# Kernel optimization log

Measured on AMD Instinct MI355X. Metric: run time of the kernel, lower is better.

Reference implementation:

```python
import jax, jax.numpy as jnp
import numpy as np
import math

K = 2
CAPACITY = -1
NEED_L_AUX = True


def topk_gating(logits, k=K, capacity=CAPACITY, need_l_aux=NEED_L_AUX):
    # logits: (T, P, E) tokens x prototypes x experts-per-prototype
    gates = jax.nn.softmax(logits.astype(jnp.float32), axis=-1).astype(logits.dtype)
    T, P, E = gates.shape
    cap = int(math.ceil(1.25 * T / E)) if capacity < 0 else capacity

    idx1 = jnp.argmax(gates, axis=-1)                      # (T, P)
    mask1 = jax.nn.one_hot(idx1, E, dtype=jnp.int32)       # (T, P, E)
    loc1 = jnp.cumsum(mask1, axis=0) - 1                   # position in expert queue
    if need_l_aux:
        me = jnp.mean(gates, axis=0)
        ce = jnp.mean(mask1.astype(jnp.float32), axis=0)
        l_aux = jnp.mean(me * ce)
    else:
        l_aux = jnp.zeros((), jnp.float32)
    mask1 = mask1 * (loc1 < cap)                           # drop over-capacity tokens
    loc1_s = jnp.sum(loc1 * mask1, axis=-1)                # (T, P)
    gates1_s = jnp.sum(gates * mask1, axis=-1)
    denom = gates1_s
    gates_s_list = [gates1_s]
    mask_list = [mask1]
    loc_s_list = [loc1_s]
    last_logits = logits
    last_mask = mask1
    prev_masks = mask1
    for _ in range(2, k + 1):
        last_logits = jnp.where(last_mask.astype(bool), -jnp.inf, last_logits)
        idx = jnp.argmax(last_logits, axis=-1)
        mask = jax.nn.one_hot(idx, E, dtype=jnp.int32)
        loc = jnp.cumsum(mask, axis=0) - 1 + jnp.sum(prev_masks, axis=0, keepdims=True)
        mask = mask * (loc < cap)
        last_mask = mask
        prev_masks = prev_masks + mask
        mask_list.append(mask)
        loc_s_list.append(jnp.sum(loc * mask, axis=-1))
        gs = jnp.sum(gates * mask, axis=-1)
        denom = denom + gs
        gates_s_list.append(gs)
    denom = jnp.maximum(denom, jnp.finfo(denom.dtype).eps)

    combine = jnp.zeros((T, P, E, cap), gates.dtype)
    for gs, mask, ls in zip(gates_s_list, mask_list, loc_s_list):
        g = (gs / denom)[..., None] * mask                  # (T, P, E)
        loc_sc = jax.nn.one_hot(ls, cap, dtype=gates.dtype)  # (T, P, cap)
        combine = combine + g[..., None] * loc_sc[:, :, None, :]
    dispatch_mask = combine.astype(bool)
    return l_aux.astype(logits.dtype), combine.astype(logits.dtype), dispatch_mask


def setup_inputs() -> dict:
    key = jax.random.key(0)
    k1, k2 = jax.random.split(key)
    inp = jax.random.normal(k1, (4096, 2048), dtype=jnp.float32)
    W = jax.random.normal(k2, (64, 2048), dtype=jnp.float32) / math.sqrt(2048.0)
    return {"input": inp, "W": W, "bs": 4096, "prototypes": 2}


def reference(input, W, bs, prototypes):
    logits = input @ W.T                                   # (T, num_experts_total)
    logits = logits.reshape(input.shape[0], prototypes, -1)  # (T, P, E)
    return topk_gating(logits, k=K, capacity=CAPACITY, need_l_aux=NEED_L_AUX)
```

## Files before the change

kernel.cpp:

```cpp
#include <hip/hip_runtime.h>
#include <cstdint>

#define T_TOK 4096
#define KDIM 2048
#define NE 64
#define NP 2
#define EE 32
#define CAP 160
#define NKC 8
#define KCHUNK 256
#define BLKR 128
#define COMB_ELEMS 41943040ull
#define OUT_ELEMS 83886081ull
#define SMALLF 65536
#define NFB 4096
#define TOT4 20971520

__global__ __launch_bounds__(256) void k_fused(const float* __restrict__ x,
                                               const float* __restrict__ W,
                                               float* __restrict__ part,
                                               float* __restrict__ out,
                                               int s1lo, int s1hi, int s2lo, int s2hi,
                                               int fillLast) {
  __shared__ float xs[BLKR][36];
  __shared__ float wt[32][68];
  const int tid = threadIdx.x;
  if (blockIdx.x >= 256) {
    const int fb = blockIdx.x - 256;
    float4* p4 = reinterpret_cast<float4*>(out);
    const float4 z4 = make_float4(0.f, 0.f, 0.f, 0.f);
    const int start = fb * 5120;
#pragma unroll
    for (int j = 0; j < 20; ++j) {
      const int i4 = start + tid + j * 256;
      if (i4 >= s1lo && i4 < s1hi) continue;
      if (i4 >= s2lo && i4 < s2hi) continue;
      p4[i4] = z4;
    }
    if (fillLast && fb == NFB - 1 && tid == 255) out[OUT_ELEMS - 1] = 0.f;
    return;
  }
  const int rb = blockIdx.x & 31;
  const int kc = blockIdx.x >> 5;
  const int r0 = rb * BLKR;
  const int er = tid & 15;
  const int rg = tid >> 4;
  float acc[8][4];
#pragma unroll
  for (int i = 0; i < 8; ++i)
#pragma unroll
    for (int c = 0; c < 4; ++c) acc[i][c] = 0.f;

  float4 sx[4], sw[2];
  {
    const int kb = kc * KCHUNK;
#pragma unroll
    for (int q = 0; q < 4; ++q) {
      const int li = tid + q * 256, row = li >> 3, kq = (li & 7) * 4;
      sx[q] = *reinterpret_cast<const float4*>(&x[(size_t)(r0 + row) * KDIM + kb + kq]);
    }
#pragma unroll
    for (int q = 0; q < 2; ++q) {
      const int li = tid + q * 256, e = li >> 3, kq = (li & 7) * 4;
      sw[q] = *reinterpret_cast<const float4*>(&W[(size_t)e * KDIM + kb + kq]);
    }
  }
  for (int s = 0; s < 8; ++s) {
    __syncthreads();
#pragma unroll
    for (int q = 0; q < 4; ++q) {
      const int li = tid + q * 256, row = li >> 3, kq = (li & 7) * 4;
      *reinterpret_cast<float4*>(&xs[row][kq]) = sx[q];
    }
#pragma unroll
    for (int q = 0; q < 2; ++q) {
      const int li = tid + q * 256, e = li >> 3, kq = (li & 7) * 4;
      wt[kq][e] = sw[q].x; wt[kq + 1][e] = sw[q].y;
      wt[kq + 2][e] = sw[q].z; wt[kq + 3][e] = sw[q].w;
    }
    if (s < 7) {
      const int kb = kc * KCHUNK + (s + 1) * 32;
#pragma unroll
      for (int q = 0; q < 4; ++q) {
        const int li = tid + q * 256, row = li >> 3, kq = (li & 7) * 4;
        sx[q] = *reinterpret_cast<const float4*>(&x[(size_t)(r0 + row) * KDIM + kb + kq]);
      }
#pragma unroll
      for (int q = 0; q < 2; ++q) {
        const int li = tid + q * 256, e = li >> 3, kq = (li & 7) * 4;
        sw[q] = *reinterpret_cast<const float4*>(&W[(size_t)e * KDIM + kb + kq]);
      }
    }
    __syncthreads();
#pragma unroll
    for (int k4 = 0; k4 < 8; ++k4) {
      float4 wb[4];
#pragma unroll
      for (int j = 0; j < 4; ++j)
        wb[j] = *reinterpret_cast<const float4*>(&wt[k4 * 4 + j][er * 4]);
#pragma unroll
      for (int i = 0; i < 8; ++i) {
        const float4 xv = *reinterpret_cast<const float4*>(&xs[rg + 16 * i][k4 * 4]);
        acc[i][0] = fmaf(xv.w, wb[3].x, fmaf(xv.z, wb[2].x, fmaf(xv.y, wb[1].x, fmaf(xv.x, wb[0].x, acc[i][0]))));
        acc[i][1] = fmaf(xv.w, wb[3].y, fmaf(xv.z, wb[2].y, fmaf(xv.y, wb[1].y, fmaf(xv.x, wb[0].y, acc[i][1]))));
        acc[i][2] = fmaf(xv.w, wb[3].z, fmaf(xv.z, wb[2].z, fmaf(xv.y, wb[1].z, fmaf(xv.x, wb[0].z, acc[i][2]))));
        acc[i][3] = fmaf(xv.w, wb[3].w, fmaf(xv.z, wb[2].w, fmaf(xv.y, wb[1].w, fmaf(xv.x, wb[0].w, acc[i][3]))));
      }
    }
  }
#pragma unroll
  for (int i = 0; i < 8; ++i) {
    float4 v; v.x = acc[i][0]; v.y = acc[i][1]; v.z = acc[i][2]; v.w = acc[i][3];
    *reinterpret_cast<float4*>(
        &part[((size_t)kc * T_TOK + r0 + rg + 16 * i) * NE + er * 4]) = v;
  }
}

__global__ __launch_bounds__(256) void k_fill2(float* __restrict__ out) {
  float4* p4 = reinterpret_cast<float4*>(out + 4);
  const float4 z4 = make_float4(0.f, 0.f, 0.f, 0.f);
  const int base = blockIdx.x * 2048 + threadIdx.x;
#pragma unroll
  for (int j = 0; j < 8; ++j) p4[base + j * 256] = z4;
}

__global__ __launch_bounds__(64) void k_soft(const float* __restrict__ part,
                                             float2* __restrict__ g12,
                                             int* __restrict__ idxs,
                                             float* __restrict__ me_part) {
  __shared__ float lg[64][33];
  const int tid = threadIdx.x;
  const int R = blockIdx.x * 64 + tid;
  const int t = R >> 1;
  const int p = R & 1;
  float v[32];
  const float* pr = part + (size_t)t * NE + p * EE;
#pragma unroll
  for (int e = 0; e < 32; e += 4) {
    float4 s = *reinterpret_cast<const float4*>(pr + e);
    v[e] = s.x; v[e + 1] = s.y; v[e + 2] = s.z; v[e + 3] = s.w;
  }
  for (int kc = 1; kc < NKC; ++kc) {
    const float* prk = pr + (size_t)kc * T_TOK * NE;
#pragma unroll
    for (int e = 0; e < 32; e += 4) {
      float4 s = *reinterpret_cast<const float4*>(prk + e);
      v[e] += s.x; v[e + 1] += s.y; v[e + 2] += s.z; v[e + 3] += s.w;
    }
  }
  float m = v[0];
#pragma unroll
  for (int e = 1; e < 32; ++e) m = fmaxf(m, v[e]);
  float sum = 0.f;
#pragma unroll
  for (int e = 0; e < 32; ++e) { v[e] = expf(v[e] - m); sum += v[e]; }
  const float inv = 1.0f / sum;
#pragma unroll
  for (int e = 0; e < 32; ++e) v[e] *= inv;
  float g1 = -1.f; int i1 = 0;
#pragma unroll
  for (int e = 0; e < 32; ++e) if (v[e] > g1) { g1 = v[e]; i1 = e; }
  float g2 = -1.f; int i2 = 0;
#pragma unroll
  for (int e = 0; e < 32; ++e) if (e != i1 && v[e] > g2) { g2 = v[e]; i2 = e; }
  g12[R] = make_float2(g1, g2);
  idxs[R] = i1 | (i2 << 8);
#pragma unroll
  for (int e = 0; e < 32; ++e) lg[tid][e] = v[e];
  __syncthreads();
  {
    const int pp = tid >> 5, ee = tid & 31;
    float s = 0.f;
    for (int rr = pp; rr < 64; rr += 2) s += lg[rr][ee];
    me_part[blockIdx.x * 64 + tid] = s;
  }
}

__global__ __launch_bounds__(1024) void k_scan(const int* __restrict__ idxs,
                                               const float2* __restrict__ g12,
                                               const float* __restrict__ me_part,
                                               int2* __restrict__ fl,
                                               float2* __restrict__ wvp,
                                               float* __restrict__ out) {
  __shared__ int grp[NP][64][32];
  __shared__ int tot[NP][32];
  __shared__ unsigned short tk1[NP][T_TOK];
  __shared__ unsigned short tk2[NP][T_TOK];
  __shared__ float red[64];
  const int tid = threadIdx.x;
  const int wvi = tid >> 6;
  const int p = wvi >> 3;
  const int wg = wvi & 7;
  const int l = tid & 63;
  const unsigned long long lmask = (1ull << l) - 1ull;
  for (int gi = 0; gi < 8; ++gi) {
    const int g = wg * 8 + gi;
    const int t = g * 64 + l;
    const int e1 = idxs[t * 2 + p] & 255;
    if (l < 32) grp[p][g][l] = 0;
    unsigned long long m = ~0ull;
#pragma unroll
    for (int b = 0; b < 5; ++b) {
      const unsigned long long bm = __ballot((e1 >> b) & 1);
      m &= ((e1 >> b) & 1) ? bm : ~bm;
    }
    const int rank = (int)__popcll(m & lmask);
    if (rank == 0) grp[p][g][e1] = (int)__popcll(m);
    tk1[p][t] = (unsigned short)(rank | (e1 << 6));
  }
  __syncthreads();
  if (tid < 64) {
    const int pp = tid >> 5, ee = tid & 31;
    int s = 0;
    for (int g = 0; g < 64; ++g) { int vv = grp[pp][g][ee]; grp[pp][g][ee] = s; s += vv; }
    tot[pp][ee] = s;
  }
  __syncthreads();
  for (int gi = 0; gi < 8; ++gi) {
    const int g = wg * 8 + gi;
    const int t = g * 64 + l;
    const int vv = tk1[p][t];
    tk1[p][t] = (unsigned short)(grp[p][g][vv >> 6] + (vv & 63));
  }
  if (tid < 64) {
    float s = 0.f;
    for (int b = 0; b < 128; ++b) s += me_part[b * 64 + tid];
    red[tid] = s * (float)tot[tid >> 5][tid & 31];
  }
  __syncthreads();
  if (tid == 0) {
    float s = 0.f;
    for (int i = 0; i < 64; ++i) s += red[i];
    out[0] = s / (64.0f * 4096.0f * 4096.0f);
  }
  for (int gi = 0; gi < 8; ++gi) {
    const int g = wg * 8 + gi;
    const int t = g * 64 + l;
    const int ii = idxs[t * 2 + p];
    const int e2 = (tk1[p][t] < CAP) ? (ii >> 8) : (ii & 255);
    if (l < 32) grp[p][g][l] = 0;
    unsigned long long m = ~0ull;
#pragma unroll
    for (int b = 0; b < 5; ++b) {
      const unsigned long long bm = __ballot((e2 >> b) & 1);
      m &= ((e2 >> b) & 1) ? bm : ~bm;
    }
    const int rank = (int)__popcll(m & lmask);
    if (rank == 0) grp[p][g][e2] = (int)__popcll(m);
    tk2[p][t] = (unsigned short)(rank | (e2 << 6));
  }
  __syncthreads();
  if (tid < 64) {
    const int pp = tid >> 5, ee = tid & 31;
    int s = min(tot[pp][ee], CAP);
    for (int g = 0; g < 64; ++g) { int vv = grp[pp][g][ee]; grp[pp][g][ee] = s; s += vv; }
  }
  __syncthreads();
  for (int gi = 0; gi < 8; ++gi) {
    const int g = wg * 8 + gi;
    const int t = g * 64 + l;
    const int R = t * 2 + p;
    const int ii = idxs[R];
    const int e1 = ii & 255;
    const int loc1v = tk1[p][t];
    const bool kept1 = loc1v < CAP;
    const int v2 = tk2[p][t];
    const int rank2 = v2 & 63, e2 = v2 >> 6;
    const int loc2 = grp[p][g][e2] + rank2;
    const bool kept2 = loc2 < CAP;
    const float2 gg = g12[R];
    const float gs1 = kept1 ? gg.x : 0.f;
    const float g2v = kept1 ? gg.y : gg.x;
    const float gs2 = kept2 ? g2v : 0.f;
    const float den = fmaxf(gs1 + gs2, 1.1920929e-07f);
    fl[R] = make_int2(kept1 ? e1 * CAP + loc1v : -1, kept2 ? e2 * CAP + loc2 : -1);
    wvp[R] = make_float2(gs1 / den, gs2 / den);
  }
}

__global__ __launch_bounds__(256) void k_fix(const int2* __restrict__ fl,
                                             const float2* __restrict__ wvp,
                                             float* __restrict__ out,
                                             int rlimit) {
  const int R = blockIdx.x * 256 + threadIdx.x;
  const int2 f = fl[R];
  const float2 w = wvp[R];
  float* oc = out + 1 + (size_t)R * 5120;
  if (f.x >= 0) oc[f.x] = w.x;
  if (f.y >= 0) oc[f.y] = w.y;
  if (R < rlimit) {
    float* od = out + 1 + COMB_ELEMS + (size_t)R * 5120;
    if (f.x >= 0) od[f.x] = 1.0f;
    if (f.y >= 0) od[f.y] = 1.0f;
  }
}

__global__ __launch_bounds__(1024) void k_write_tail(const int2* __restrict__ fl,
                                                     float* __restrict__ out,
                                                     int nfullB) {
  __shared__ int2 sfl[16];
  const int tid = threadIdx.x;
  const int rstart = nfullB * 2;
  const int nr = 8192 - rstart;
  if (tid < nr) sfl[tid] = fl[rstart + tid];
  __syncthreads();
  const size_t base = 1 + COMB_ELEMS + (size_t)rstart * 5120;
  const int cnt = nr * 5120;
  const int nx4 = (cnt - 4) >> 2;
  float4* p4 = (float4*)(out + base + 3);
  const float4 z4 = make_float4(0.f, 0.f, 0.f, 0.f);
  for (int idx = tid; idx < nx4; idx += 1024) p4[idx] = z4;
  if (tid < 3) out[base + tid] = 0.f;
  if (tid == 3) out[base + cnt - 1] = 0.f;
  __syncthreads();
  if (tid < 2 * nr) {
    const int rr = rstart + (tid >> 1);
    const int2 f = sfl[tid >> 1];
    const int pos = (tid & 1) ? f.y : f.x;
    if (pos >= 0) out[1 + COMB_ELEMS + (size_t)rr * 5120 + pos] = 1.0f;
  }
}

extern "C" void kernel_launch(void* const* d_in, const int* in_sizes, int n_in,
                              void* d_out, int out_size, void* d_ws, size_t ws_size,
                              hipStream_t stream) {
  const float* x = (const float*)d_in[0];
  const float* W = (const float*)d_in[1];
  float* out = (float*)d_out;

  const size_t PARTF = (size_t)NKC * T_TOK * NE;

  float* small;
  float* part;
  int s1lo = 0, s1hi = 0, s2lo = 0, s2hi = 0, fillLast = 1;
  bool needFill2 = false;
  int nfullB = 4096, rlimit = 8192;
  if (ws_size >= (SMALLF + PARTF) * sizeof(float)) {
    small = (float*)d_ws;
    part = small + SMALLF;
  } else if (ws_size >= SMALLF * sizeof(float)) {
    small = (float*)d_ws;
    part = out + 4;
    s1lo = 1; s1hi = 1 + (int)(PARTF / 4);
    needFill2 = true;
  } else {
    const size_t tb = (OUT_ELEMS - SMALLF) & ~(size_t)3;
    small = out + tb;
    part = out + 4;
    s1lo = 1; s1hi = 1 + (int)(PARTF / 4);
    s2lo = (int)(tb / 4); s2hi = TOT4;
    fillLast = 0;
    needFill2 = true;
    nfullB = (int)((tb - 1 - COMB_ELEMS) / 10240);
    rlimit = nfullB * 2;
  }
  float2* g12 = (float2*)small;
  int* idxs = (int*)(small + 16384);
  float* me_part = small + 24576;
  int2* fl = (int2*)(small + 32768);
  float2* wvp = (float2*)(small + 49152);

  hipLaunchKernelGGL(k_fused, dim3(256 + NFB), dim3(256), 0, stream,
                     x, W, part, out, s1lo, s1hi, s2lo, s2hi, fillLast);
  hipLaunchKernelGGL(k_soft, dim3(128), dim3(64), 0, stream, part, g12, idxs, me_part);
  if (needFill2)
    hipLaunchKernelGGL(k_fill2, dim3(256), dim3(256), 0, stream, out);
  hipLaunchKernelGGL(k_scan, dim3(1), dim3(1024), 0, stream, idxs, g12, me_part, fl, wvp, out);
  hipLaunchKernelGGL(k_fix, dim3(32), dim3(256), 0, stream, fl, wvp, out, rlimit);
  if (nfullB < 4096)
    hipLaunchKernelGGL(k_write_tail, dim3(1), dim3(1024), 0, stream, fl, out, nfullB);
}
```

Measured before the change: 104.0 us.

## Fuse softmax into GEMM via last-block ticket and fold scatter into scan

The softmax/top-2 kernel moves into the GEMM kernel. A per-row-block atomic ticket lets the last of the 8 K-chunk blocks reduce the partials and compute gates, and it writes 32 per-block me partials instead of 128. The scatter of combine and dispatch entries moves into the single-block scan kernel, removing the separate fix kernel. A memset of tickets is added, and the fallback workspace paths are reworked, including placing partials near the end of the output. This removes two launches and their gaps, at the cost of a serial tail in the winning blocks and scattered writes now done by only one block.

Result: slower. 164.1 us (+57.8%).

```diff
diff --git a/kernel.cpp b/kernel.cpp
--- a/kernel.cpp
+++ b/kernel.cpp
@@ -12,21 +12,26 @@
 #define BLKR 128
 #define COMB_ELEMS 41943040ull
 #define OUT_ELEMS 83886081ull
-#define SMALLF 65536
+#define PARTF 2097152ull
+#define TOT4 20971520
 #define NFB 4096
-#define TOT4 20971520
-
-__global__ __launch_bounds__(256) void k_fused(const float* __restrict__ x,
-                                               const float* __restrict__ W,
-                                               float* __restrict__ part,
-                                               float* __restrict__ out,
-                                               int s1lo, int s1hi, int s2lo, int s2hi,
-                                               int fillLast) {
-  __shared__ float xs[BLKR][36];
-  __shared__ float wt[32][68];
+#define SMALLF 59424
+#define PB_F 81788928
+
+__global__ __launch_bounds__(256)
+void k_mega(const float* __restrict__ x, const float* __restrict__ W,
+            float* __restrict__ part, float2* __restrict__ g12,
+            int* __restrict__ idxs, float* __restrict__ me_part,
+            float* __restrict__ out, unsigned int* __restrict__ tickets,
+            int s1lo, int s1hi, int s2lo, int s2hi, int fillLast) {
+  __shared__ union {
+    struct { float xs[BLKR][36]; float wt[32][68]; } g;
+    float lg[256][33];
+  } sh;
+  __shared__ int iswin;
   const int tid = threadIdx.x;
   if (blockIdx.x >= 256) {
-    const int fb = blockIdx.x - 256;
+    const int fb = (int)blockIdx.x - 256;
     float4* p4 = reinterpret_cast<float4*>(out);
     const float4 z4 = make_float4(0.f, 0.f, 0.f, 0.f);
     const int start = fb * 5120;
@@ -40,8 +45,8 @@
     if (fillLast && fb == NFB - 1 && tid == 255) out[OUT_ELEMS - 1] = 0.f;
     return;
   }
-  const int rb = blockIdx.x & 31;
-  const int kc = blockIdx.x >> 5;
+  const int rb = (int)blockIdx.x & 31;
+  const int kc = (int)blockIdx.x >> 5;
   const int r0 = rb * BLKR;
   const int er = tid & 15;
   const int rg = tid >> 4;
@@ -50,7 +55,6 @@
   for (int i = 0; i < 8; ++i)
 #pragma unroll
     for (int c = 0; c < 4; ++c) acc[i][c] = 0.f;
-
   float4 sx[4], sw[2];
   {
     const int kb = kc * KCHUNK;
@@ -70,13 +74,13 @@
 #pragma unroll
     for (int q = 0; q < 4; ++q) {
       const int li = tid + q * 256, row = li >> 3, kq = (li & 7) * 4;
-      *reinterpret_cast<float4*>(&xs[row][kq]) = sx[q];
+      *reinterpret_cast<float4*>(&sh.g.xs[row][kq]) = sx[q];
     }
 #pragma unroll
     for (int q = 0; q < 2; ++q) {
       const int li = tid + q * 256, e = li >> 3, kq = (li & 7) * 4;
-      wt[kq][e] = sw[q].x; wt[kq + 1][e] = sw[q].y;
-      wt[kq + 2][e] = sw[q].z; wt[kq + 3][e] = sw[q].w;
+      sh.g.wt[kq][e] = sw[q].x; sh.g.wt[kq + 1][e] = sw[q].y;
+      sh.g.wt[kq + 2][e] = sw[q].z; sh.g.wt[kq + 3][e] = sw[q].w;
     }
     if (s < 7) {
       const int kb = kc * KCHUNK + (s + 1) * 32;
@@ -97,10 +101,10 @@
       float4 wb[4];
 #pragma unroll
       for (int j = 0; j < 4; ++j)
-        wb[j] = *reinterpret_cast<const float4*>(&wt[k4 * 4 + j][er * 4]);
+        wb[j] = *reinterpret_cast<const float4*>(&sh.g.wt[k4 * 4 + j][er * 4]);
 #pragma unroll
       for (int i = 0; i < 8; ++i) {
-        const float4 xv = *reinterpret_cast<const float4*>(&xs[rg + 16 * i][k4 * 4]);
+        const float4 xv = *reinterpret_cast<const float4*>(&sh.g.xs[rg + 16 * i][k4 * 4]);
         acc[i][0] = fmaf(xv.w, wb[3].x, fmaf(xv.z, wb[2].x, fmaf(xv.y, wb[1].x, fmaf(xv.x, wb[0].x, acc[i][0]))));
         acc[i][1] = fmaf(xv.w, wb[3].y, fmaf(xv.z, wb[2].y, fmaf(xv.y, wb[1].y, fmaf(xv.x, wb[0].y, acc[i][1]))));
         acc[i][2] = fmaf(xv.w, wb[3].z, fmaf(xv.z, wb[2].z, fmaf(xv.y, wb[1].z, fmaf(xv.x, wb[0].z, acc[i][2]))));
@@ -114,74 +118,67 @@
     *reinterpret_cast<float4*>(
         &part[((size_t)kc * T_TOK + r0 + rg + 16 * i) * NE + er * 4]) = v;
   }
-}
-
-__global__ __launch_bounds__(256) void k_fill2(float* __restrict__ out) {
-  float4* p4 = reinterpret_cast<float4*>(out + 4);
-  const float4 z4 = make_float4(0.f, 0.f, 0.f, 0.f);
-  const int base = blockIdx.x * 2048 + threadIdx.x;
-#pragma unroll
-  for (int j = 0; j < 8; ++j) p4[base + j * 256] = z4;
-}
-
-__global__ __launch_bounds__(64) void k_soft(const float* __restrict__ part,
-                                             float2* __restrict__ g12,
-                                             int* __restrict__ idxs,
-                                             float* __restrict__ me_part) {
-  __shared__ float lg[64][33];
-  const int tid = threadIdx.x;
-  const int R = blockIdx.x * 64 + tid;
-  const int t = R >> 1;
-  const int p = R & 1;
-  float v[32];
-  const float* pr = part + (size_t)t * NE + p * EE;
-#pragma unroll
-  for (int e = 0; e < 32; e += 4) {
-    float4 s = *reinterpret_cast<const float4*>(pr + e);
-    v[e] = s.x; v[e + 1] = s.y; v[e + 2] = s.z; v[e + 3] = s.w;
-  }
-  for (int kc = 1; kc < NKC; ++kc) {
-    const float* prk = pr + (size_t)kc * T_TOK * NE;
+  __threadfence();
+  if (tid == 0) iswin = (atomicAdd(&tickets[rb], 1u) == 7u);
+  __syncthreads();
+  if (!iswin) return;
+  __threadfence();
+  {
+    const int row = tid >> 1, p = tid & 1;
+    const int t = r0 + row;
+    const int R = t * 2 + p;
+    float v[32];
+    const float* pr = part + (size_t)t * NE + p * EE;
 #pragma unroll
     for (int e = 0; e < 32; e += 4) {
-      float4 s = *reinterpret_cast<const float4*>(prk + e);
-      v[e] += s.x; v[e + 1] += s.y; v[e + 2] += s.z; v[e + 3] += s.w;
-    }
-  }
-  float m = v[0];
-#pragma unroll
-  for (int e = 1; e < 32; ++e) m = fmaxf(m, v[e]);
-  float sum = 0.f;
-#pragma unroll
-  for (int e = 0; e < 32; ++e) { v[e] = expf(v[e] - m); sum += v[e]; }
-  const float inv = 1.0f / sum;
-#pragma unroll
-  for (int e = 0; e < 32; ++e) v[e] *= inv;
-  float g1 = -1.f; int i1 = 0;
-#pragma unroll
-  for (int e = 0; e < 32; ++e) if (v[e] > g1) { g1 = v[e]; i1 = e; }
-  float g2 = -1.f; int i2 = 0;
-#pragma unroll
-  for (int e = 0; e < 32; ++e) if (e != i1 && v[e] > g2) { g2 = v[e]; i2 = e; }
-  g12[R] = make_float2(g1, g2);
-  idxs[R] = i1 | (i2 << 8);
-#pragma unroll
-  for (int e = 0; e < 32; ++e) lg[tid][e] = v[e];
-  __syncthreads();
-  {
+      const float4 sv = *reinterpret_cast<const float4*>(pr + e);
+      v[e] = sv.x; v[e + 1] = sv.y; v[e + 2] = sv.z; v[e + 3] = sv.w;
+    }
+    for (int kc2 = 1; kc2 < NKC; ++kc2) {
+      const float* prk = pr + (size_t)kc2 * T_TOK * NE;
+#pragma unroll
+      for (int e = 0; e < 32; e += 4) {
+        const float4 sv = *reinterpret_cast<const float4*>(prk + e);
+        v[e] += sv.x; v[e + 1] += sv.y; v[e + 2] += sv.z; v[e + 3] += sv.w;
+      }
+    }
+    float m = v[0];
+#pragma unroll
+    for (int e = 1; e < 32; ++e) m = fmaxf(m, v[e]);
+    float sum = 0.f;
+#pragma unroll
+    for (int e = 0; e < 32; ++e) { v[e] = expf(v[e] - m); sum += v[e]; }
+    const float inv = 1.0f / sum;
+#pragma unroll
+    for (int e = 0; e < 32; ++e) v[e] *= inv;
+    float g1 = -1.f; int i1 = 0;
+#pragma unroll
+    for (int e = 0; e < 32; ++e) if (v[e] > g1) { g1 = v[e]; i1 = e; }
+    float g2 = -1.f; int i2 = 0;
+#pragma unroll
+    for (int e = 0; e < 32; ++e) if (e != i1 && v[e] > g2) { g2 = v[e]; i2 = e; }
+    g12[R] = make_float2(g1, g2);
+    idxs[R] = i1 | (i2 << 8);
+    __syncthreads();
+#pragma unroll
+    for (int e = 0; e < 32; ++e) sh.lg[tid][e] = v[e];
+  }
+  __syncthreads();
+  if (tid < 64) {
     const int pp = tid >> 5, ee = tid & 31;
     float s = 0.f;
-    for (int rr = pp; rr < 64; rr += 2) s += lg[rr][ee];
-    me_part[blockIdx.x * 64 + tid] = s;
-  }
-}
-
-__global__ __launch_bounds__(1024) void k_scan(const int* __restrict__ idxs,
-                                               const float2* __restrict__ g12,
-                                               const float* __restrict__ me_part,
-                                               int2* __restrict__ fl,
-                                               float2* __restrict__ wvp,
-                                               float* __restrict__ out) {
+    for (int rr = 0; rr < 128; ++rr) s += sh.lg[rr * 2 + pp][ee];
+    me_part[rb * 64 + tid] = s;
+  }
+}
+
+__global__ __launch_bounds__(1024) void k_scan2(const int* __restrict__ idxs,
+                                                const float2* __restrict__ g12,
+                                                const float* __restrict__ me_part,
+                                                int2* __restrict__ fl,
+                                                float2* __restrict__ wvp,
+                                                float* __restrict__ out,
+                                                int rlimit) {
   __shared__ int grp[NP][64][32];
   __shared__ int tot[NP][32];
   __shared__ unsigned short tk1[NP][T_TOK];
@@ -224,7 +221,7 @@
   }
   if (tid < 64) {
     float s = 0.f;
-    for (int b = 0; b < 128; ++b) s += me_part[b * 64 + tid];
+    for (int b = 0; b < 32; ++b) s += me_part[b * 64 + tid];
     red[tid] = s * (float)tot[tid >> 5][tid & 31];
   }
   __syncthreads();
@@ -273,31 +270,42 @@
     const float g2v = kept1 ? gg.y : gg.x;
     const float gs2 = kept2 ? g2v : 0.f;
     const float den = fmaxf(gs1 + gs2, 1.1920929e-07f);
-    fl[R] = make_int2(kept1 ? e1 * CAP + loc1v : -1, kept2 ? e2 * CAP + loc2 : -1);
-    wvp[R] = make_float2(gs1 / den, gs2 / den);
-  }
-}
-
-__global__ __launch_bounds__(256) void k_fix(const int2* __restrict__ fl,
-                                             const float2* __restrict__ wvp,
-                                             float* __restrict__ out,
-                                             int rlimit) {
-  const int R = blockIdx.x * 256 + threadIdx.x;
-  const int2 f = fl[R];
-  const float2 w = wvp[R];
-  float* oc = out + 1 + (size_t)R * 5120;
-  if (f.x >= 0) oc[f.x] = w.x;
-  if (f.y >= 0) oc[f.y] = w.y;
-  if (R < rlimit) {
-    float* od = out + 1 + COMB_ELEMS + (size_t)R * 5120;
-    if (f.x >= 0) od[f.x] = 1.0f;
-    if (f.y >= 0) od[f.y] = 1.0f;
-  }
-}
-
-__global__ __launch_bounds__(1024) void k_write_tail(const int2* __restrict__ fl,
-                                                     float* __restrict__ out,
-                                                     int nfullB) {
+    const int f1 = kept1 ? e1 * CAP + loc1v : -1;
+    const int f2 = kept2 ? e2 * CAP + loc2 : -1;
+    const float w1 = gs1 / den, w2 = gs2 / den;
+    fl[R] = make_int2(f1, f2);
+    wvp[R] = make_float2(w1, w2);
+    float* oc = out + 1 + (size_t)R * 5120;
+    if (f1 >= 0) oc[f1] = w1;
+    if (f2 >= 0) oc[f2] = w2;
+    if (R < rlimit) {
+      float* od = out + 1 + COMB_ELEMS + (size_t)R * 5120;
+      if (f1 >= 0) od[f1] = 1.0f;
+      if (f2 >= 0) od[f2] = 1.0f;
+    }
+  }
+}
+
+__global__ __launch_bounds__(256) void k_tailB(float* __restrict__ out) {
+  float4* p4 = reinterpret_cast<float4*>(out);
+  const float4 z4 = make_float4(0.f, 0.f, 0.f, 0.f);
+  const int base = 20447232 + (int)blockIdx.x * 4096 + (int)threadIdx.x;
+#pragma unroll
+  for (int j = 0; j < 16; ++j) p4[base + j * 256] = z4;
+  if (blockIdx.x == 0 && threadIdx.x == 0) out[OUT_ELEMS - 1] = 0.f;
+}
+
+__global__ __launch_bounds__(256) void k_fill2C(float* __restrict__ out) {
+  float4* p4 = reinterpret_cast<float4*>(out + 4);
+  const float4 z4 = make_float4(0.f, 0.f, 0.f, 0.f);
+  const int base = (int)blockIdx.x * 2048 + (int)threadIdx.x;
+#pragma unroll
+  for (int j = 0; j < 8; ++j) p4[base + j * 256] = z4;
+}
+
+__global__ __launch_bounds__(1024) void k_tailC(const int2* __restrict__ fl,
+                                                float* __restrict__ out,
+                                                int nfullB) {
   __shared__ int2 sfl[16];
   const int tid = threadIdx.x;
   const int rstart = nfullB * 2;
@@ -328,21 +336,21 @@
   const float* W = (const float*)d_in[1];
   float* out = (float*)d_out;
 
-  const size_t PARTF = (size_t)NKC * T_TOK * NE;
+  const bool pathA = ws_size >= (SMALLF + PARTF) * sizeof(float);
+  const bool pathB = !pathA && ws_size >= SMALLF * sizeof(float);
 
   float* small;
   float* part;
   int s1lo = 0, s1hi = 0, s2lo = 0, s2hi = 0, fillLast = 1;
-  bool needFill2 = false;
-  int nfullB = 4096, rlimit = 8192;
-  if (ws_size >= (SMALLF + PARTF) * sizeof(float)) {
+  int rlimit = 8192, nfullB = 4096;
+  if (pathA) {
     small = (float*)d_ws;
     part = small + SMALLF;
-  } else if (ws_size >= SMALLF * sizeof(float)) {
+  } else if (pathB) {
     small = (float*)d_ws;
-    part = out + 4;
-    s1lo = 1; s1hi = 1 + (int)(PARTF / 4);
-    needFill2 = true;
+    part = out + PB_F;
+    s1lo = PB_F / 4; s1hi = TOT4;
+    fillLast = 0;
   } else {
     const size_t tb = (OUT_ELEMS - SMALLF) & ~(size_t)3;
     small = out + tb;
@@ -350,23 +358,26 @@
     s1lo = 1; s1hi = 1 + (int)(PARTF / 4);
     s2lo = (int)(tb / 4); s2hi = TOT4;
     fillLast = 0;
-    needFill2 = true;
     nfullB = (int)((tb - 1 - COMB_ELEMS) / 10240);
     rlimit = nfullB * 2;
   }
   float2* g12 = (float2*)small;
   int* idxs = (int*)(small + 16384);
   float* me_part = small + 24576;
-  int2* fl = (int2*)(small + 32768);
-  float2* wvp = (float2*)(small + 49152);
-
-  hipLaunchKernelGGL(k_fused, dim3(256 + NFB), dim3(256), 0, stream,
-                     x, W, part, out, s1lo, s1hi, s2lo, s2hi, fillLast);
-  hipLaunchKernelGGL(k_soft, dim3(128), dim3(64), 0, stream, part, g12, idxs, me_part);
-  if (needFill2)
-    hipLaunchKernelGGL(k_fill2, dim3(256), dim3(256), 0, stream, out);
-  hipLaunchKernelGGL(k_scan, dim3(1), dim3(1024), 0, stream, idxs, g12, me_part, fl, wvp, out);
-  hipLaunchKernelGGL(k_fix, dim3(32), dim3(256), 0, stream, fl, wvp, out, rlimit);
-  if (nfullB < 4096)
-    hipLaunchKernelGGL(k_write_tail, dim3(1), dim3(1024), 0, stream, fl, out, nfullB);
-}
+  int2* fl = (int2*)(small + 26624);
+  float2* wvp = (float2*)(small + 43008);
+  unsigned int* tickets = (unsigned int*)(small + 59392);
+
+  hipMemsetAsync(tickets, 0, 32 * sizeof(unsigned int), stream);
+  hipLaunchKernelGGL(k_mega, dim3(256 + NFB), dim3(256), 0, stream,
+                     x, W, part, g12, idxs, me_part, out, tickets,
+                     s1lo, s1hi, s2lo, s2hi, fillLast);
+  if (pathB)
+    hipLaunchKernelGGL(k_tailB, dim3(128), dim3(256), 0, stream, out);
+  if (!pathA && !pathB)
+    hipLaunchKernelGGL(k_fill2C, dim3(256), dim3(256), 0, stream, out);
+  hipLaunchKernelGGL(k_scan2, dim3(1), dim3(1024), 0, stream,
+                     idxs, g12, me_part, fl, wvp, out, rlimit);
+  if (!pathA && !pathB)
+    hipLaunchKernelGGL(k_tailC, dim3(1), dim3(1024), 0, stream, fl, out, nfullB);
+}
```
